# Kernel tuning notes

Hardware: AMD Instinct MI355X
Metric: run time of the kernel (lower is better)

## Reference

```python
import jax, jax.numpy as jnp
import numpy as np

D_MODEL = 128
D_STATE = 64
VOCAB_SIZE = 2000
LN_EPS = 1e-5


def setup_inputs() -> dict:
    key = jax.random.key(0)
    ks = jax.random.split(key, 8)
    B, L = 32, 4096
    x = jax.random.randint(ks[0], (B, L), 0, VOCAB_SIZE, dtype=jnp.int64)
    emb = jax.random.normal(ks[1], (VOCAB_SIZE, D_MODEL), dtype=jnp.float32)
    ln_w = jnp.ones((D_MODEL,), dtype=jnp.float32)
    ln_b = jnp.zeros((D_MODEL,), dtype=jnp.float32)
    # S4D params, initialized as in the torch module
    A_log = jnp.log(jnp.arange(1, D_STATE + 1, dtype=jnp.float32))
    D = jax.random.normal(ks[2], (D_MODEL,), dtype=jnp.float32)
    # C is complex64 in torch, but exp(at) is purely real so only Re(C) affects K
    C_re = jax.random.normal(ks[3], (D_MODEL, D_STATE), dtype=jnp.float32)
    log_dt = jnp.log(jnp.full((D_MODEL,), 0.01, dtype=jnp.float32))
    W_cls = jax.random.normal(ks[4], (2, D_MODEL), dtype=jnp.float32) * 0.02
    b_cls = jnp.zeros((2,), dtype=jnp.float32)
    return {"x": x, "emb": emb, "ln_w": ln_w, "ln_b": ln_b,
            "A_log": A_log, "D": D, "C_re": C_re, "log_dt": log_dt,
            "W_cls": W_cls, "b_cls": b_cls}


def _layernorm(h, w, b):
    mu = jnp.mean(h, axis=-1, keepdims=True)
    var = jnp.mean((h - mu) ** 2, axis=-1, keepdims=True)
    return (h - mu) * jax.lax.rsqrt(var + LN_EPS) * w + b


def _s4d(u, A_log, D, C_re, log_dt):
    # u: [B, L, M]
    L = u.shape[1]
    dt = jnp.exp(log_dt)                      # [M]
    A = -jnp.exp(A_log)                       # [N]
    t = jnp.arange(L, dtype=u.dtype)          # [L]
    # at: [M, L, N] = dt_m * A_n * t_l  (real; torch casts to complex64 but imag=0)
    at = dt[:, None, None] * A[None, None, :] * t[None, :, None]
    K = jnp.einsum('mn,mln->ml', C_re, jnp.exp(at))  # [M, L]
    # FFT causal convolution with zero padding to 2L
    u_t = jnp.swapaxes(u, 1, 2)               # [B, M, L]
    u_f = jnp.fft.rfft(u_t, n=2 * L)          # [B, M, L+1]
    k_f = jnp.fft.rfft(K, n=2 * L)            # [M, L+1]
    y = jnp.fft.irfft(u_f * k_f[None], n=2 * L)[..., :L]  # [B, M, L]
    return jnp.swapaxes(y, 1, 2) + u * D


def reference(x, emb, ln_w, ln_b, A_log, D, C_re, log_dt, W_cls, b_cls):
    h = emb[x]                                 # [B, L, M]
    h = _layernorm(h, ln_w, ln_b)
    h = _s4d(h, A_log, D, C_re, log_dt)        # [B, L, M]
    pooled = jnp.mean(h, axis=1)               # [B, M]
    return pooled @ W_cls.T + b_cls            # [B, 2]
```

## Files before the change

### kernel.cpp

```cpp
#include <hip/hip_runtime.h>
#include <math.h>

#define D_MODEL 128
#define D_STATE 64
#define VOCAB 2000
#define SEQ_L 4096
#define BATCH 32
#define JSPLIT 64
#define CHUNK (SEQ_L / JSPLIT)
#define SEG 32
#define SEGH 16
#define LN_BLOCKS (VOCAB / 4)
#define W_BLOCKS (SEQ_L / SEG)
#define LN_EPS 1e-5f

__global__ __launch_bounds__(256) void prep_kernel(
    const float* __restrict__ emb, const float* __restrict__ ln_w,
    const float* __restrict__ ln_b, const float* __restrict__ A_log,
    const float* __restrict__ Dp, const float* __restrict__ C_re,
    const float* __restrict__ log_dt, float* __restrict__ e_ln,
    float* __restrict__ Wv) {
  if (blockIdx.x < LN_BLOCKS) {
    int v = blockIdx.x * 4 + (threadIdx.x >> 6);
    int t = threadIdx.x & 63;
    const float* row = emb + v * D_MODEL;
    float h0 = row[t];
    float h1 = row[t + 64];
    float s = h0 + h1;
#pragma unroll
    for (int off = 32; off; off >>= 1) s += __shfl_xor(s, off);
    float mu = s * (1.0f / D_MODEL);
    float d0 = h0 - mu, d1 = h1 - mu;
    float q = d0 * d0 + d1 * d1;
#pragma unroll
    for (int off = 32; off; off >>= 1) q += __shfl_xor(q, off);
    float var = q * (1.0f / D_MODEL);
    float rs = rsqrtf(var + LN_EPS);
    e_ln[v * D_MODEL + t]      = d0 * rs * ln_w[t]      + ln_b[t];
    e_ln[v * D_MODEL + t + 64] = d1 * rs * ln_w[t + 64] + ln_b[t + 64];
  } else {
    __shared__ float Ash[D_STATE];
    if (threadIdx.x < D_STATE) Ash[threadIdx.x] = -expf(A_log[threadIdx.x]);
    __syncthreads();
    int wb = blockIdx.x - LN_BLOCKS;
    int m = threadIdx.x & (D_MODEL - 1);
    int sub = threadIdx.x >> 7;
    int j0 = wb * SEG + sub * SEGH;
    float acc[SEGH];
#pragma unroll
    for (int k = 0; k < SEGH; ++k) acc[k] = 0.0f;
    float dt = expf(log_dt[m]);
    float bs = 0.0f;
    float r1_end = (float)(SEQ_L - j0 - (SEGH - 1));
    for (int n = 0; n < D_STATE; ++n) {
      float x = dt * Ash[n];
      float q = expf(x);
      float r = C_re[m * D_STATE + n] / (1.0f - q);
      bs += r;
      float g = expf(x * r1_end);
      acc[SEGH - 1] += r * g;
#pragma unroll
      for (int jj = SEGH - 2; jj >= 0; --jj) {
        g *= q;
        acc[jj] += r * g;
      }
    }
    float base = Dp[m] + bs;
#pragma unroll
    for (int k = 0; k < SEGH; ++k)
      Wv[(j0 + k) * D_MODEL + m] = base - acc[k];
  }
}

__global__ __launch_bounds__(128) void reduce_kernel(
    const int* __restrict__ x, const float* __restrict__ e_ln,
    const float* __restrict__ Wv, float* __restrict__ part) {
  __shared__ int toks[CHUNK];
  int b = blockIdx.x;
  int sIdx = blockIdx.y;
  int m = threadIdx.x;
  if (m < CHUNK) toks[m] = x[b * SEQ_L + sIdx * CHUNK + m];
  __syncthreads();
  const float* wbase = Wv + sIdx * CHUNK * D_MODEL + m;
  float a0 = 0.0f, a1 = 0.0f, a2 = 0.0f, a3 = 0.0f;
#pragma unroll
  for (int j = 0; j < CHUNK; j += 4) {
    int t0 = toks[j], t1 = toks[j + 1], t2 = toks[j + 2], t3 = toks[j + 3];
    float e0 = e_ln[t0 * D_MODEL + m];
    float e1 = e_ln[t1 * D_MODEL + m];
    float e2 = e_ln[t2 * D_MODEL + m];
    float e3 = e_ln[t3 * D_MODEL + m];
    float w0 = wbase[(j + 0) * D_MODEL];
    float w1 = wbase[(j + 1) * D_MODEL];
    float w2 = wbase[(j + 2) * D_MODEL];
    float w3 = wbase[(j + 3) * D_MODEL];
    a0 = fmaf(e0, w0, a0);
    a1 = fmaf(e1, w1, a1);
    a2 = fmaf(e2, w2, a2);
    a3 = fmaf(e3, w3, a3);
  }
  part[(b * JSPLIT + sIdx) * D_MODEL + m] = (a0 + a1) + (a2 + a3);
}

__global__ __launch_bounds__(64) void final_kernel(
    const float* __restrict__ part, const float* __restrict__ W_cls,
    const float* __restrict__ b_cls, float* __restrict__ out) {
  int b = blockIdx.x;
  int t = threadIdx.x;
  float p1 = 0.0f, p2 = 0.0f;
#pragma unroll 4
  for (int s = 0; s < JSPLIT; ++s) {
    p1 += part[(b * JSPLIT + s) * D_MODEL + t];
    p2 += part[(b * JSPLIT + s) * D_MODEL + t + 64];
  }
  p1 *= (1.0f / SEQ_L);
  p2 *= (1.0f / SEQ_L);
  float c0 = p1 * W_cls[t]           + p2 * W_cls[t + 64];
  float c1 = p1 * W_cls[D_MODEL + t] + p2 * W_cls[D_MODEL + t + 64];
#pragma unroll
  for (int off = 32; off; off >>= 1) {
    c0 += __shfl_xor(c0, off);
    c1 += __shfl_xor(c1, off);
  }
  if (t == 0) {
    out[b * 2 + 0] = c0 + b_cls[0];
    out[b * 2 + 1] = c1 + b_cls[1];
  }
}

extern "C" void kernel_launch(void* const* d_in, const int* in_sizes, int n_in,
                              void* d_out, int out_size, void* d_ws, size_t ws_size,
                              hipStream_t stream) {
  const int*   x      = (const int*)d_in[0];
  const float* emb    = (const float*)d_in[1];
  const float* ln_w   = (const float*)d_in[2];
  const float* ln_b   = (const float*)d_in[3];
  const float* A_log  = (const float*)d_in[4];
  const float* Dp     = (const float*)d_in[5];
  const float* C_re   = (const float*)d_in[6];
  const float* log_dt = (const float*)d_in[7];
  const float* W_cls  = (const float*)d_in[8];
  const float* b_cls  = (const float*)d_in[9];
  float* out = (float*)d_out;

  char* ws = (char*)d_ws;
  float* e_ln = (float*)(ws);
  float* Wv   = (float*)(ws + 1048576);
  float* part = (float*)(ws + 3145728);

  prep_kernel<<<LN_BLOCKS + W_BLOCKS, 256, 0, stream>>>(
      emb, ln_w, ln_b, A_log, Dp, C_re, log_dt, e_ln, Wv);
  reduce_kernel<<<dim3(BATCH, JSPLIT), 128, 0, stream>>>(x, e_ln, Wv, part);
  final_kernel<<<BATCH, 64, 0, stream>>>(part, W_cls, b_cls, out);
}
```

Baseline: 30.94 us.

## Fuse reduce and final classifier into one per-batch 1024-thread kernel

Replaces the two-stage reduction (a 32x64 grid of 128-thread partial-sum blocks plus a separate final kernel) with one 1024-thread block per batch row. Each block loads the whole token row into shared memory, eight groups each cover a slice of the sequence, and the classifier dot product and cross-wave reduction are folded in through shuffles and shared memory. This drops a kernel launch and the partial-sum round trip through global memory. In exchange only 32 blocks run, so most of the GPU's compute units sit idle and each thread walks a 512-step serial loop, which may leave too little parallelism to hide gather latency.

```diff
diff --git a/kernel.cpp b/kernel.cpp
--- a/kernel.cpp
+++ b/kernel.cpp
@@ -6,12 +6,12 @@
 #define VOCAB 2000
 #define SEQ_L 4096
 #define BATCH 32
-#define JSPLIT 64
-#define CHUNK (SEQ_L / JSPLIT)
 #define SEG 32
 #define SEGH 16
 #define LN_BLOCKS (VOCAB / 4)
 #define W_BLOCKS (SEQ_L / SEG)
+#define JGRP 8
+#define JPER (SEQ_L / JGRP)
 #define LN_EPS 1e-5f
 
 __global__ __launch_bounds__(256) void prep_kernel(
@@ -72,59 +72,65 @@
   }
 }
 
-__global__ __launch_bounds__(128) void reduce_kernel(
+__global__ __launch_bounds__(1024) void batch_reduce_kernel(
     const int* __restrict__ x, const float* __restrict__ e_ln,
-    const float* __restrict__ Wv, float* __restrict__ part) {
-  __shared__ int toks[CHUNK];
+    const float* __restrict__ Wv, const float* __restrict__ W_cls,
+    const float* __restrict__ b_cls, float* __restrict__ out) {
+  __shared__ int toks[SEQ_L];
+  __shared__ float sm[16][2];
   int b = blockIdx.x;
-  int sIdx = blockIdx.y;
-  int m = threadIdx.x;
-  if (m < CHUNK) toks[m] = x[b * SEQ_L + sIdx * CHUNK + m];
+  int tid = threadIdx.x;
+  const int* xrow = x + b * SEQ_L;
+#pragma unroll
+  for (int i = 0; i < SEQ_L / 1024; ++i)
+    toks[tid + i * 1024] = xrow[tid + i * 1024];
   __syncthreads();
-  const float* wbase = Wv + sIdx * CHUNK * D_MODEL + m;
+  int m = tid & (D_MODEL - 1);
+  int grp = tid >> 7;
+  int j0 = grp * JPER;
   float a0 = 0.0f, a1 = 0.0f, a2 = 0.0f, a3 = 0.0f;
-#pragma unroll
-  for (int j = 0; j < CHUNK; j += 4) {
+#pragma unroll 4
+  for (int j = j0; j < j0 + JPER; j += 4) {
     int t0 = toks[j], t1 = toks[j + 1], t2 = toks[j + 2], t3 = toks[j + 3];
     float e0 = e_ln[t0 * D_MODEL + m];
     float e1 = e_ln[t1 * D_MODEL + m];
     float e2 = e_ln[t2 * D_MODEL + m];
     float e3 = e_ln[t3 * D_MODEL + m];
-    float w0 = wbase[(j + 0) * D_MODEL];
-    float w1 = wbase[(j + 1) * D_MODEL];
-    float w2 = wbase[(j + 2) * D_MODEL];
-    float w3 = wbase[(j + 3) * D_MODEL];
+    float w0 = Wv[(j + 0) * D_MODEL + m];
+    float w1 = Wv[(j + 1) * D_MODEL + m];
+    float w2 = Wv[(j + 2) * D_MODEL + m];
+    float w3 = Wv[(j + 3) * D_MODEL + m];
     a0 = fmaf(e0, w0, a0);
     a1 = fmaf(e1, w1, a1);
     a2 = fmaf(e2, w2, a2);
     a3 = fmaf(e3, w3, a3);
   }
-  part[(b * JSPLIT + sIdx) * D_MODEL + m] = (a0 + a1) + (a2 + a3);
-}
-
-__global__ __launch_bounds__(64) void final_kernel(
-    const float* __restrict__ part, const float* __restrict__ W_cls,
-    const float* __restrict__ b_cls, float* __restrict__ out) {
-  int b = blockIdx.x;
-  int t = threadIdx.x;
-  float p1 = 0.0f, p2 = 0.0f;
-#pragma unroll 4
-  for (int s = 0; s < JSPLIT; ++s) {
-    p1 += part[(b * JSPLIT + s) * D_MODEL + t];
-    p2 += part[(b * JSPLIT + s) * D_MODEL + t + 64];
-  }
-  p1 *= (1.0f / SEQ_L);
-  p2 *= (1.0f / SEQ_L);
-  float c0 = p1 * W_cls[t]           + p2 * W_cls[t + 64];
-  float c1 = p1 * W_cls[D_MODEL + t] + p2 * W_cls[D_MODEL + t + 64];
+  float p = (a0 + a1) + (a2 + a3);
+  float v0 = p * W_cls[m];
+  float v1 = p * W_cls[D_MODEL + m];
 #pragma unroll
   for (int off = 32; off; off >>= 1) {
-    c0 += __shfl_xor(c0, off);
-    c1 += __shfl_xor(c1, off);
+    v0 += __shfl_xor(v0, off);
+    v1 += __shfl_xor(v1, off);
   }
-  if (t == 0) {
-    out[b * 2 + 0] = c0 + b_cls[0];
-    out[b * 2 + 1] = c1 + b_cls[1];
+  int wave = tid >> 6;
+  if ((tid & 63) == 0) {
+    sm[wave][0] = v0;
+    sm[wave][1] = v1;
+  }
+  __syncthreads();
+  if (tid < 16) {
+    float u0 = sm[tid][0];
+    float u1 = sm[tid][1];
+#pragma unroll
+    for (int off = 8; off; off >>= 1) {
+      u0 += __shfl_xor(u0, off);
+      u1 += __shfl_xor(u1, off);
+    }
+    if (tid == 0) {
+      out[b * 2 + 0] = u0 * (1.0f / SEQ_L) + b_cls[0];
+      out[b * 2 + 1] = u1 * (1.0f / SEQ_L) + b_cls[1];
+    }
   }
 }
 
@@ -146,10 +152,9 @@
   char* ws = (char*)d_ws;
   float* e_ln = (float*)(ws);
   float* Wv   = (float*)(ws + 1048576);
-  float* part = (float*)(ws + 3145728);
 
   prep_kernel<<<LN_BLOCKS + W_BLOCKS, 256, 0, stream>>>(
       emb, ln_w, ln_b, A_log, Dp, C_re, log_dt, e_ln, Wv);
-  reduce_kernel<<<dim3(BATCH, JSPLIT), 128, 0, stream>>>(x, e_ln, Wv, part);
-  final_kernel<<<BATCH, 64, 0, stream>>>(part, W_cls, b_cls, out);
+  batch_reduce_kernel<<<BATCH, 1024, 0, stream>>>(
+      x, e_ln, Wv, W_cls, b_cls, out);
 }
```

After: 59.45 us. 92.2% more time.
